# Optimization experiments

Hardware: AMD Instinct MI355X
Metric: run time of the kernel (lower is better)

Reference implementation:

```python
import jax, jax.numpy as jnp
import numpy as np

N_CLASSES = 16384
M = 2
D = 128


def setup_inputs() -> dict:
    key = jax.random.key(0)
    k1, k2 = jax.random.split(key)
    x = jax.random.normal(k1, (N_CLASSES * M, D), dtype=jnp.float32)
    anchor_idx = jax.random.randint(k2, (N_CLASSES,), 0, M, dtype=jnp.int64 if jax.config.jax_enable_x64 else jnp.int32).astype(jnp.int32)
    pos_idx = (1 - anchor_idx).astype(jnp.int32)  # randperm(2) -> positive is the other sample
    return {"x": x, "anchor_idx": anchor_idx, "pos_idx": pos_idx}


def reference(x, anchor_idx, pos_idx):
    # x: [N*M, D]; anchor_idx/pos_idx: [N] in [0, M)
    N = anchor_idx.shape[0]
    Dx = x.shape[1]
    xr = x.reshape(N, M, Dx)
    anchors = jnp.take_along_axis(xr, anchor_idx[:, None, None], axis=1)[:, 0, :]    # [N, D]
    positives = jnp.take_along_axis(xr, pos_idx[:, None, None], axis=1)[:, 0, :]     # [N, D]
    negs = xr[:, 1, :]                                                               # [N, D] (sample 1 of every class)
    # score[i, j] = a_i . (neg_j - pos_i) = a_i . neg_j - a_i . pos_i
    S = anchors @ negs.T                                                             # [N, N]
    ap = jnp.sum(anchors * positives, axis=1)                                        # [N]
    logits = S - ap[:, None]
    mask = ~jnp.eye(N, dtype=bool)                                                   # exclude j == i (own class)
    sums = jnp.sum(jnp.where(mask, jnp.exp(logits), jnp.float32(0.0)), axis=1)       # [N]
    return jnp.sum(jnp.log1p(sums))
```

## Files before the change

### kernel.cpp

```cpp
#include <hip/hip_runtime.h>
#include <hip/hip_bf16.h>
#include <math.h>

#define N_CLS 16384
#define DDIM  128
#define CSHIFT 50.0f
#define LOG2E 1.4426950408889634f
#define NEGC2 (-72.13475204444817f)

#if __has_builtin(__builtin_amdgcn_exp2f)
#define EXP2(x) __builtin_amdgcn_exp2f(x)
#else
#define EXP2(x) exp2f(x)
#endif

typedef __attribute__((ext_vector_type(8))) short short8;
typedef __attribute__((ext_vector_type(4))) float f32x4;

__device__ __forceinline__ unsigned short f2bf(float f) {
    __hip_bfloat16 h = __float2bfloat16(f);
    return *(unsigned short*)&h;
}

__global__ __launch_bounds__(256)
void prep_kernel(const float* __restrict__ x,
                 const int* __restrict__ aidx,
                 float* __restrict__ ap,
                 unsigned short* __restrict__ Afrag,
                 unsigned short* __restrict__ Bfrag,
                 float* __restrict__ out) {
    const int t = threadIdx.x;
    const int tl = blockIdx.x;
    const int kc = t >> 6, q = (t >> 4) & 3, m = t & 15;
    const int col = kc * 32 + q * 8;
    const int i = tl * 16 + m;

    float fa[8], fb[8];
    *(float4*)&fa[0] = *(const float4*)(x + (2L * i) * DDIM + col);
    *(float4*)&fa[4] = *(const float4*)(x + (2L * i) * DDIM + col + 4);
    *(float4*)&fb[0] = *(const float4*)(x + (2L * i + 1) * DDIM + col);
    *(float4*)&fb[4] = *(const float4*)(x + (2L * i + 1) * DDIM + col + 4);
    const bool sel = (aidx[i] != 0);

    short8 As8, Bs8;
    float d = 0.0f;
    #pragma unroll
    for (int j = 0; j < 8; ++j) {
        const float av = sel ? fb[j] : fa[j];
        As8[j] = (short)f2bf(av * LOG2E);
        Bs8[j] = (short)f2bf(fb[j]);
        d += fa[j] * fb[j];
    }
    *(short8*)(Afrag + (long)tl * 2048 + t * 8) = As8;
    *(short8*)(Bfrag + (long)tl * 2048 + t * 8) = Bs8;

    d += __shfl_xor(d, 16, 64);
    d += __shfl_xor(d, 32, 64);
    __shared__ float sap[4][16];
    if ((t & 63) < 16) sap[kc][t & 63] = d;
    __syncthreads();
    if (t < 16) ap[tl * 16 + t] = sap[0][t] + sap[1][t] + sap[2][t] + sap[3][t];
    if (t == 0 && tl == 0) out[0] = 0.0f;
}

__global__ __launch_bounds__(256, 2)
void fused_kernel(const unsigned short* __restrict__ Afrag,
                  const unsigned short* __restrict__ Bfrag,
                  float* __restrict__ partial) {
    const int tid = threadIdx.x;
    const int lane = tid & 63;
    const int w = tid >> 6;
    const int quad = lane >> 4;
    const int l15 = lane & 15;
    const int oct = blockIdx.x & 7;
    const int rt = blockIdx.x >> 3;
    const int wm2 = w >> 1;
    const int wh = w & 1;

    short8 af[4][4];
    {
        const unsigned short* abase =
            Afrag + ((long)(rt * 8 + wm2 * 4) * 4) * 512 + lane * 8;
        #pragma unroll
        for (int mt = 0; mt < 4; ++mt)
            #pragma unroll
            for (int kc = 0; kc < 4; ++kc)
                af[mt][kc] = *(const short8*)(abase + (mt * 4 + kc) * 512);
    }

    const unsigned short* bbase =
        Bfrag + ((long)(oct * 128 + wh * 4) * 4) * 512 + lane * 8;

    const f32x4 cinit = (f32x4){NEGC2, NEGC2, NEGC2, NEGC2};
    float rs[4][4] = {};
    short8 bP[4], bQ[4];
    f32x4 accA[4], accB[4];

    const bool canDiag = ((rt >> 4) == oct) && (wm2 == wh);
    const int itd = canDiag ? (rt & 15) : -1;

    auto mfma4 = [&](f32x4 (&acc)[4], short8 (&b)[4]) {
        #pragma unroll
        for (int mt = 0; mt < 4; ++mt)
            acc[mt] = __builtin_amdgcn_mfma_f32_16x16x32_bf16(
                af[mt][0], b[0], cinit, 0, 0, 0);
        #pragma unroll
        for (int kc = 1; kc < 4; ++kc)
            #pragma unroll
            for (int mt = 0; mt < 4; ++mt)
                acc[mt] = __builtin_amdgcn_mfma_f32_16x16x32_bf16(
                    af[mt][kc], b[kc], acc[mt], 0, 0, 0);
    };
    auto epi = [&](f32x4 (&acc)[4]) {
        #pragma unroll
        for (int mt = 0; mt < 4; ++mt)
            #pragma unroll
            for (int reg = 0; reg < 4; ++reg)
                rs[mt][reg] += EXP2(acc[mt][reg]);
    };
    auto epiD = [&](f32x4 (&acc)[4], int nt) {
        #pragma unroll
        for (int mt = 0; mt < 4; ++mt)
            #pragma unroll
            for (int reg = 0; reg < 4; ++reg) {
                float e = EXP2(acc[mt][reg]);
                if (mt == nt) e = (quad * 4 + reg == l15) ? 0.0f : e;
                rs[mt][reg] += e;
            }
    };

    #pragma unroll
    for (int kc = 0; kc < 4; ++kc)
        bP[kc] = *(const short8*)(bbase + kc * 512);

    bool dprev = false;
    for (int it = 0; it < 16; ++it) {
        const unsigned short* p1 = bbase + (long)it * 16384;
        const bool d = (it == itd);

        #pragma unroll
        for (int kc = 0; kc < 4; ++kc)
            bQ[kc] = *(const short8*)(p1 + 2048 + kc * 512);
        mfma4(accA, bP);
        if (it > 0) { if (dprev) epiD(accB, 3); else epi(accB); }

        #pragma unroll
        for (int kc = 0; kc < 4; ++kc)
            bP[kc] = *(const short8*)(p1 + 4096 + kc * 512);
        mfma4(accB, bQ);
        if (d) epiD(accA, 0); else epi(accA);

        #pragma unroll
        for (int kc = 0; kc < 4; ++kc)
            bQ[kc] = *(const short8*)(p1 + 6144 + kc * 512);
        mfma4(accA, bP);
        if (d) epiD(accB, 1); else epi(accB);

        const unsigned short* p2 = bbase + (long)((it < 15) ? it + 1 : it) * 16384;
        #pragma unroll
        for (int kc = 0; kc < 4; ++kc)
            bP[kc] = *(const short8*)(p2 + kc * 512);
        mfma4(accB, bQ);
        if (d) epiD(accA, 2); else epi(accA);

        dprev = d;
    }
    if (dprev) epiD(accB, 3); else epi(accB);

    const int slot = oct * 2 + wh;
    const int rowBase = rt * 128 + wm2 * 64;
    #pragma unroll
    for (int mt = 0; mt < 4; ++mt)
        #pragma unroll
        for (int reg = 0; reg < 4; ++reg) {
            float v = rs[mt][reg];
            v += __shfl_xor(v, 1, 64);
            v += __shfl_xor(v, 2, 64);
            v += __shfl_xor(v, 4, 64);
            v += __shfl_xor(v, 8, 64);
            if (l15 == 0)
                partial[(long)slot * N_CLS + rowBase + mt * 16 + quad * 4 + reg] = v;
        }
}

__global__ __launch_bounds__(256)
void finalize_kernel(const float* __restrict__ partial,
                     const float* __restrict__ ap,
                     float* __restrict__ out) {
    __shared__ float red[256];
    const int t = threadIdx.x;
    const int row = blockIdx.x * 256 + t;
    float s = 0.0f;
    #pragma unroll
    for (int p = 0; p < 16; ++p) s += partial[(long)p * N_CLS + row];
    const float u = logf(s) + (CSHIFT - ap[row]);
    const float loss = (u > 25.0f) ? u : log1pf(__expf(u));
    red[t] = loss;
    __syncthreads();
    for (int st = 128; st > 0; st >>= 1) {
        if (t < st) red[t] += red[t + st];
        __syncthreads();
    }
    if (t == 0) atomicAdd(out, red[0]);
}

extern "C" void kernel_launch(void* const* d_in, const int* in_sizes, int n_in,
                              void* d_out, int out_size, void* d_ws, size_t ws_size,
                              hipStream_t stream) {
    const float* x    = (const float*)d_in[0];
    const int*   aidx = (const int*)d_in[1];

    char* ws = (char*)d_ws;
    float* ap             = (float*)(ws);
    float* partial        = (float*)(ws + 131072);
    unsigned short* Afrag = (unsigned short*)(ws + 131072 + 1048576);
    unsigned short* Bfrag = (unsigned short*)(ws + 131072 + 1048576 + 4194304);

    prep_kernel<<<N_CLS / 16, 256, 0, stream>>>(x, aidx, ap, Afrag, Bfrag, (float*)d_out);
    fused_kernel<<<1024, 256, 0, stream>>>(Afrag, Bfrag, partial);
    finalize_kernel<<<64, 256, 0, stream>>>(partial, ap, (float*)d_out);
}
```

Before: 136.4 us.

## Switch to 32x32x16 MFMA with per-wave 32-row tiles and new fragment layout

Replaces the 16x16x32 bf16 MFMA tiling (each wave 64 rows x 64 cols, two ping-pong accumulators) with 32x32x16 MFMA where each wave owns a 32-row strip and walks 64 column tiles with a single 16-float accumulator. The prep kernel is rewritten to emit operand fragments in the 32x32 layout, and the exp shift constant is removed so accumulators start at zero. Occupancy hint rises to 4 blocks per SU and partial sums drop from 16 to 8 slots. This aims to cut register pressure and MFMA instruction count, but it drops the overflow-guarding shift and the interleaving of MFMA with exp work.

Result: slower. 154.9 us (+13.6%).

```diff
diff --git a/kernel.cpp b/kernel.cpp
--- a/kernel.cpp
+++ b/kernel.cpp
@@ -4,9 +4,7 @@
 
 #define N_CLS 16384
 #define DDIM  128
-#define CSHIFT 50.0f
 #define LOG2E 1.4426950408889634f
-#define NEGC2 (-72.13475204444817f)
 
 #if __has_builtin(__builtin_amdgcn_exp2f)
 #define EXP2(x) __builtin_amdgcn_exp2f(x)
@@ -15,7 +13,7 @@
 #endif
 
 typedef __attribute__((ext_vector_type(8))) short short8;
-typedef __attribute__((ext_vector_type(4))) float f32x4;
+typedef __attribute__((ext_vector_type(16))) float f32x16;
 
 __device__ __forceinline__ unsigned short f2bf(float f) {
     __hip_bfloat16 h = __float2bfloat16(f);
@@ -30,157 +28,124 @@
                  unsigned short* __restrict__ Bfrag,
                  float* __restrict__ out) {
     const int t = threadIdx.x;
-    const int tl = blockIdx.x;
-    const int kc = t >> 6, q = (t >> 4) & 3, m = t & 15;
-    const int col = kc * 32 + q * 8;
-    const int i = tl * 16 + m;
-
-    float fa[8], fb[8];
-    *(float4*)&fa[0] = *(const float4*)(x + (2L * i) * DDIM + col);
-    *(float4*)&fa[4] = *(const float4*)(x + (2L * i) * DDIM + col + 4);
-    *(float4*)&fb[0] = *(const float4*)(x + (2L * i + 1) * DDIM + col);
-    *(float4*)&fb[4] = *(const float4*)(x + (2L * i + 1) * DDIM + col + 4);
+    const int g = blockIdx.x;
+    const int lane = t & 63;
+    const int w = t >> 6;
+    const int m = lane & 31;
+    const int half = lane >> 5;
+    const int i = g * 32 + m;
     const bool sel = (aidx[i] != 0);
 
-    short8 As8, Bs8;
     float d = 0.0f;
     #pragma unroll
-    for (int j = 0; j < 8; ++j) {
-        const float av = sel ? fb[j] : fa[j];
-        As8[j] = (short)f2bf(av * LOG2E);
-        Bs8[j] = (short)f2bf(fb[j]);
-        d += fa[j] * fb[j];
+    for (int h = 0; h < 2; ++h) {
+        const int kc = w * 2 + h;
+        const int k0 = kc * 16 + half * 8;
+        float fa[8], fb[8];
+        *(float4*)&fa[0] = *(const float4*)(x + (2L * i) * DDIM + k0);
+        *(float4*)&fa[4] = *(const float4*)(x + (2L * i) * DDIM + k0 + 4);
+        *(float4*)&fb[0] = *(const float4*)(x + (2L * i + 1) * DDIM + k0);
+        *(float4*)&fb[4] = *(const float4*)(x + (2L * i + 1) * DDIM + k0 + 4);
+        short8 As8, Bs8;
+        #pragma unroll
+        for (int j = 0; j < 8; ++j) {
+            const float av = sel ? fb[j] : fa[j];
+            As8[j] = (short)f2bf(av * LOG2E);
+            Bs8[j] = (short)f2bf(fb[j]);
+            d += fa[j] * fb[j];
+        }
+        *(short8*)(Afrag + (long)g * 4096 + kc * 512 + lane * 8) = As8;
+        *(short8*)(Bfrag + (long)g * 4096 + kc * 512 + lane * 8) = Bs8;
     }
-    *(short8*)(Afrag + (long)tl * 2048 + t * 8) = As8;
-    *(short8*)(Bfrag + (long)tl * 2048 + t * 8) = Bs8;
-
-    d += __shfl_xor(d, 16, 64);
     d += __shfl_xor(d, 32, 64);
-    __shared__ float sap[4][16];
-    if ((t & 63) < 16) sap[kc][t & 63] = d;
+    __shared__ float sap[4][32];
+    if (lane < 32) sap[w][lane] = d;
     __syncthreads();
-    if (t < 16) ap[tl * 16 + t] = sap[0][t] + sap[1][t] + sap[2][t] + sap[3][t];
-    if (t == 0 && tl == 0) out[0] = 0.0f;
+    if (t < 32) ap[g * 32 + t] = sap[0][t] + sap[1][t] + sap[2][t] + sap[3][t];
+    if (t == 0 && g == 0) out[0] = 0.0f;
 }
 
-__global__ __launch_bounds__(256, 2)
+__global__ __launch_bounds__(256, 4)
 void fused_kernel(const unsigned short* __restrict__ Afrag,
                   const unsigned short* __restrict__ Bfrag,
                   float* __restrict__ partial) {
     const int tid = threadIdx.x;
     const int lane = tid & 63;
     const int w = tid >> 6;
-    const int quad = lane >> 4;
-    const int l15 = lane & 15;
+    const int l31 = lane & 31;
+    const int hi = lane >> 5;
     const int oct = blockIdx.x & 7;
     const int rt = blockIdx.x >> 3;
-    const int wm2 = w >> 1;
-    const int wh = w & 1;
+    const int gRow = rt * 4 + w;
 
-    short8 af[4][4];
+    short8 af[8];
     {
-        const unsigned short* abase =
-            Afrag + ((long)(rt * 8 + wm2 * 4) * 4) * 512 + lane * 8;
+        const unsigned short* abase = Afrag + (long)gRow * 4096 + lane * 8;
         #pragma unroll
-        for (int mt = 0; mt < 4; ++mt)
-            #pragma unroll
-            for (int kc = 0; kc < 4; ++kc)
-                af[mt][kc] = *(const short8*)(abase + (mt * 4 + kc) * 512);
+        for (int kc = 0; kc < 8; ++kc)
+            af[kc] = *(const short8*)(abase + kc * 512);
     }
+    const unsigned short* bbase = Bfrag + (long)oct * 64 * 4096 + lane * 8;
 
-    const unsigned short* bbase =
-        Bfrag + ((long)(oct * 128 + wh * 4) * 4) * 512 + lane * 8;
+    const int ctd0 = gRow - oct * 64;
+    const int ctd = (ctd0 >= 0 && ctd0 < 64) ? ctd0 : -1;
 
-    const f32x4 cinit = (f32x4){NEGC2, NEGC2, NEGC2, NEGC2};
-    float rs[4][4] = {};
+    float rs[16];
+    #pragma unroll
+    for (int r = 0; r < 16; ++r) rs[r] = 0.0f;
+
     short8 bP[4], bQ[4];
-    f32x4 accA[4], accB[4];
+    #pragma unroll
+    for (int kc = 0; kc < 4; ++kc) bP[kc] = *(const short8*)(bbase + kc * 512);
+    #pragma unroll
+    for (int kc = 0; kc < 4; ++kc) bQ[kc] = *(const short8*)(bbase + 2048 + kc * 512);
 
-    const bool canDiag = ((rt >> 4) == oct) && (wm2 == wh);
-    const int itd = canDiag ? (rt & 15) : -1;
+    for (int ct = 0; ct < 64; ++ct) {
+        const unsigned short* nb = bbase + (long)((ct < 63) ? ct + 1 : ct) * 4096;
 
-    auto mfma4 = [&](f32x4 (&acc)[4], short8 (&b)[4]) {
+        f32x16 acc;
         #pragma unroll
-        for (int mt = 0; mt < 4; ++mt)
-            acc[mt] = __builtin_amdgcn_mfma_f32_16x16x32_bf16(
-                af[mt][0], b[0], cinit, 0, 0, 0);
-        #pragma unroll
-        for (int kc = 1; kc < 4; ++kc)
-            #pragma unroll
-            for (int mt = 0; mt < 4; ++mt)
-                acc[mt] = __builtin_amdgcn_mfma_f32_16x16x32_bf16(
-                    af[mt][kc], b[kc], acc[mt], 0, 0, 0);
-    };
-    auto epi = [&](f32x4 (&acc)[4]) {
-        #pragma unroll
-        for (int mt = 0; mt < 4; ++mt)
-            #pragma unroll
-            for (int reg = 0; reg < 4; ++reg)
-                rs[mt][reg] += EXP2(acc[mt][reg]);
-    };
-    auto epiD = [&](f32x4 (&acc)[4], int nt) {
-        #pragma unroll
-        for (int mt = 0; mt < 4; ++mt)
-            #pragma unroll
-            for (int reg = 0; reg < 4; ++reg) {
-                float e = EXP2(acc[mt][reg]);
-                if (mt == nt) e = (quad * 4 + reg == l15) ? 0.0f : e;
-                rs[mt][reg] += e;
-            }
-    };
-
-    #pragma unroll
-    for (int kc = 0; kc < 4; ++kc)
-        bP[kc] = *(const short8*)(bbase + kc * 512);
-
-    bool dprev = false;
-    for (int it = 0; it < 16; ++it) {
-        const unsigned short* p1 = bbase + (long)it * 16384;
-        const bool d = (it == itd);
+        for (int r = 0; r < 16; ++r) acc[r] = 0.0f;
 
         #pragma unroll
         for (int kc = 0; kc < 4; ++kc)
-            bQ[kc] = *(const short8*)(p1 + 2048 + kc * 512);
-        mfma4(accA, bP);
-        if (it > 0) { if (dprev) epiD(accB, 3); else epi(accB); }
-
+            acc = __builtin_amdgcn_mfma_f32_32x32x16_bf16(af[kc], bP[kc], acc, 0, 0, 0);
         #pragma unroll
         for (int kc = 0; kc < 4; ++kc)
-            bP[kc] = *(const short8*)(p1 + 4096 + kc * 512);
-        mfma4(accB, bQ);
-        if (d) epiD(accA, 0); else epi(accA);
-
+            bP[kc] = *(const short8*)(nb + kc * 512);
         #pragma unroll
         for (int kc = 0; kc < 4; ++kc)
-            bQ[kc] = *(const short8*)(p1 + 6144 + kc * 512);
-        mfma4(accA, bP);
-        if (d) epiD(accB, 1); else epi(accB);
-
-        const unsigned short* p2 = bbase + (long)((it < 15) ? it + 1 : it) * 16384;
+            acc = __builtin_amdgcn_mfma_f32_32x32x16_bf16(af[4 + kc], bQ[kc], acc, 0, 0, 0);
         #pragma unroll
         for (int kc = 0; kc < 4; ++kc)
-            bP[kc] = *(const short8*)(p2 + kc * 512);
-        mfma4(accB, bQ);
-        if (d) epiD(accA, 2); else epi(accA);
+            bQ[kc] = *(const short8*)(nb + 2048 + kc * 512);
 
-        dprev = d;
+        if (ct == ctd) {
+            #pragma unroll
+            for (int r = 0; r < 16; ++r) {
+                const float e = EXP2(acc[r]);
+                const int row = (r & 3) + 8 * (r >> 2) + 4 * hi;
+                rs[r] += (l31 == row) ? 0.0f : e;
+            }
+        } else {
+            #pragma unroll
+            for (int r = 0; r < 16; ++r) rs[r] += EXP2(acc[r]);
+        }
     }
-    if (dprev) epiD(accB, 3); else epi(accB);
 
-    const int slot = oct * 2 + wh;
-    const int rowBase = rt * 128 + wm2 * 64;
     #pragma unroll
-    for (int mt = 0; mt < 4; ++mt)
-        #pragma unroll
-        for (int reg = 0; reg < 4; ++reg) {
-            float v = rs[mt][reg];
-            v += __shfl_xor(v, 1, 64);
-            v += __shfl_xor(v, 2, 64);
-            v += __shfl_xor(v, 4, 64);
-            v += __shfl_xor(v, 8, 64);
-            if (l15 == 0)
-                partial[(long)slot * N_CLS + rowBase + mt * 16 + quad * 4 + reg] = v;
+    for (int r = 0; r < 16; ++r) {
+        float v = rs[r];
+        v += __shfl_xor(v, 1, 64);
+        v += __shfl_xor(v, 2, 64);
+        v += __shfl_xor(v, 4, 64);
+        v += __shfl_xor(v, 8, 64);
+        v += __shfl_xor(v, 16, 64);
+        if (l31 == 0) {
+            const int row = (r & 3) + 8 * (r >> 2) + 4 * hi;
+            partial[(long)oct * N_CLS + (long)gRow * 32 + row] = v;
         }
+    }
 }
 
 __global__ __launch_bounds__(256)
@@ -192,8 +157,8 @@
     const int row = blockIdx.x * 256 + t;
     float s = 0.0f;
     #pragma unroll
-    for (int p = 0; p < 16; ++p) s += partial[(long)p * N_CLS + row];
-    const float u = logf(s) + (CSHIFT - ap[row]);
+    for (int p = 0; p < 8; ++p) s += partial[(long)p * N_CLS + row];
+    const float u = logf(s) - ap[row];
     const float loss = (u > 25.0f) ? u : log1pf(__expf(u));
     red[t] = loss;
     __syncthreads();
@@ -216,7 +181,7 @@
     unsigned short* Afrag = (unsigned short*)(ws + 131072 + 1048576);
     unsigned short* Bfrag = (unsigned short*)(ws + 131072 + 1048576 + 4194304);
 
-    prep_kernel<<<N_CLS / 16, 256, 0, stream>>>(x, aidx, ap, Afrag, Bfrag, (float*)d_out);
+    prep_kernel<<<N_CLS / 32, 256, 0, stream>>>(x, aidx, ap, Afrag, Bfrag, (float*)d_out);
     fused_kernel<<<1024, 256, 0, stream>>>(Afrag, Bfrag, partial);
     finalize_kernel<<<64, 256, 0, stream>>>(partial, ap, (float*)d_out);
 }
```
